# Performance work log

Measured on AMD Instinct MI355X. Metric: run time of the kernel, lower is better.

Reference implementation:

```python
import jax, jax.numpy as jnp
import numpy as np

K = 7
G = 16
PAD = K // 2
EPS = 1e-5


def setup_inputs() -> dict:
    key = jax.random.key(0)
    ks = jax.random.split(key, 8)
    C = 256
    Cr = C // 4  # ratio=4 bottleneck
    inputs = jax.random.normal(ks[0], (4, C, 56, 56), dtype=jnp.float32)
    W1 = jax.random.normal(ks[1], (Cr, C), dtype=jnp.float32) * 0.05
    b1 = jax.random.normal(ks[2], (Cr,), dtype=jnp.float32) * 0.05
    gamma = jax.random.normal(ks[3], (Cr,), dtype=jnp.float32) * 0.1 + 1.0
    beta = jax.random.normal(ks[4], (Cr,), dtype=jnp.float32) * 0.1
    mean = jax.random.normal(ks[5], (Cr,), dtype=jnp.float32) * 0.1
    var = jax.random.uniform(ks[6], (Cr,), dtype=jnp.float32) * 0.5 + 0.5
    W2 = jax.random.normal(ks[7], (G * K * K, Cr), dtype=jnp.float32) * 0.05
    b2 = jnp.zeros((G * K * K,), dtype=jnp.float32)
    return {"inputs": inputs, "W1": W1, "b1": b1, "gamma": gamma,
            "beta": beta, "mean": mean, "var": var, "W2": W2, "b2": b2}


def reference(inputs, W1, b1, gamma, beta, mean, var, W2, b2):
    B, C, H, W = inputs.shape
    Cg = C // G
    # kernel-generation branch: 1x1 conv -> BN (eval stats) -> relu -> 1x1 conv
    t = jnp.einsum('bchw,oc->bohw', inputs, W1) + b1[None, :, None, None]
    scale = gamma / jnp.sqrt(var + EPS)
    t = t * scale[None, :, None, None] + (beta - mean * scale)[None, :, None, None]
    t = jax.nn.relu(t)
    w = jnp.einsum('bchw,oc->bohw', t, W2) + b2[None, :, None, None]
    w = w.reshape(B, G, K * K, H, W)  # per-pixel kernel
    # involution: accumulate shifted slices instead of materializing unfold
    xp = jnp.pad(inputs, ((0, 0), (0, 0), (PAD, PAD), (PAD, PAD)))
    xg = xp.reshape(B, G, Cg, H + 2 * PAD, W + 2 * PAD)
    out = jnp.zeros((B, G, Cg, H, W), dtype=inputs.dtype)
    k = 0
    for i in range(K):
        for j in range(K):
            out = out + xg[:, :, :, i:i + H, j:j + W] * w[:, :, k][:, :, None, :, :]
            k += 1
    return out.reshape(B, C, H, W)
```

## Files before the change

kernel.cpp:

```cpp
#include <hip/hip_runtime.h>

#define HW    3136
#define HDIM  56
#define CIN   256
#define CR    64
#define NG    16
#define KK    49
#define BEPS  1e-5f
#define RB    2
#define NBAND 28
#define WSTR  116
#define XROWS 8
#define XSTR  68
#define XTOT  (XROWS * 8 * XSTR)

typedef __attribute__((ext_vector_type(8))) short short8;
typedef __attribute__((ext_vector_type(4))) float f32x4;

__device__ __forceinline__ unsigned short f2bf(float f) {
    union { float f; unsigned u; } v; v.f = f;
    unsigned r = (v.u + 0x7FFFu + ((v.u >> 16) & 1u)) >> 16;
    return (unsigned short)r;
}

__global__ __launch_bounds__(256) void k0_prep(
    const float* __restrict__ W1, const float* __restrict__ b1,
    const float* __restrict__ gamma, const float* __restrict__ beta,
    const float* __restrict__ mean, const float* __restrict__ var,
    const float* __restrict__ W2,
    unsigned short* __restrict__ W1b, unsigned short* __restrict__ W2bT,
    float* __restrict__ b1f)
{
    int idx = blockIdx.x * 256 + threadIdx.x;
    if (idx < CR * CIN) {
        int o = idx >> 8;
        float s = gamma[o] * rsqrtf(var[o] + BEPS);
        W1b[idx] = f2bf(W1[idx] * s);
    } else if (idx < CR * CIN + NG * 64 * 64) {
        int j = idx - CR * CIN;
        int c = j & 63, tap = (j >> 6) & 63, g = j >> 12;
        float v = (tap < KK) ? W2[(g * KK + tap) * CR + c] : 0.f;
        W2bT[j] = f2bf(v);
    } else if (idx < CR * CIN + NG * 64 * 64 + CR) {
        int o = idx - CR * CIN - NG * 64 * 64;
        float s = gamma[o] * rsqrtf(var[o] + BEPS);
        b1f[o] = b1[o] * s + beta[o] - mean[o] * s;
    }
}

__global__ __launch_bounds__(256) void k1_gemm(
    const float* __restrict__ x, const unsigned short* __restrict__ W1b,
    const float* __restrict__ b1f, unsigned short* __restrict__ t_bf)
{
    const int tid = threadIdx.x;
    const int b = blockIdx.y;
    const int lane = tid & 63, l15 = lane & 15, q = lane >> 4;
    const int wid = tid >> 6;
    const int pxb = blockIdx.x * 64 + wid * 16;

    const float* xp = x + (size_t)b * CIN * HW + pxb + l15;

    f32x4 acc[4];
#pragma unroll
    for (int nt = 0; nt < 4; nt++) acc[nt] = (f32x4){0.f, 0.f, 0.f, 0.f};

#pragma unroll 2
    for (int kc = 0; kc < 8; kc++) {
        short8 af;
#pragma unroll
        for (int j = 0; j < 8; j++) {
            float xv = xp[(size_t)(kc * 32 + q * 8 + j) * HW];
            af[j] = (short)f2bf(xv);
        }
#pragma unroll
        for (int nt = 0; nt < 4; nt++) {
            short8 bf = *(const short8*)&W1b[(size_t)(16 * nt + l15) * CIN + kc * 32 + q * 8];
            acc[nt] = __builtin_amdgcn_mfma_f32_16x16x32_bf16(af, bf, acc[nt], 0, 0, 0);
        }
    }
#pragma unroll
    for (int nt = 0; nt < 4; nt++) {
        float bias = b1f[16 * nt + l15];
#pragma unroll
        for (int r = 0; r < 4; r++) {
            int px = pxb + 4 * q + r;
            float v = fmaxf(acc[nt][r] + bias, 0.f);
            t_bf[((size_t)b * HW + px) * CR + 16 * nt + l15] = f2bf(v);
        }
    }
}

__global__ __launch_bounds__(256, 4) void k2_fused(
    const float* __restrict__ x, const unsigned short* __restrict__ t_bf,
    const unsigned short* __restrict__ W2bT, const float* __restrict__ b2,
    float* __restrict__ out)
{
    __shared__ float w_lds[KK * WSTR];
    __shared__ float x_lds[XTOT];

    const int tid = threadIdx.x;
    const int band = blockIdx.x, g = blockIdx.y;
    const int b = blockIdx.z >> 1, half = blockIdx.z & 1;
    const int h0 = band * RB;
    const int lane = tid & 63, l15 = lane & 15, q = lane >> 4;
    const int wid = tid >> 6;

#pragma unroll
    for (int it = 0; it < 17; it++) {
        int i = it * 256 + tid;
        int col = i % XSTR; int t2 = i / XSTR; int cg = t2 & 7; int rowx = t2 >> 3;
        int hy = h0 - 3 + rowx, xc = col - 4;
        float v = 0.f;
        if (hy >= 0 && hy < HDIM && xc >= 0 && xc < HDIM)
            v = x[((size_t)b * CIN + g * 16 + half * 8 + cg) * HW + hy * HDIM + xc];
        x_lds[i] = v;
    }

    {
        short8 bfr[4][2];
#pragma unroll
        for (int nt = 0; nt < 4; nt++)
#pragma unroll
            for (int ks = 0; ks < 2; ks++)
                bfr[nt][ks] = *(const short8*)&W2bT[((size_t)g * 64 + 16 * nt + l15) * 64 + ks * 32 + q * 8];
        float b2v[4];
#pragma unroll
        for (int nt = 0; nt < 4; nt++) {
            int tap = 16 * nt + l15;
            b2v[nt] = (tap < KK) ? b2[g * KK + tap] : 0.f;
        }
#pragma unroll
        for (int it = 0; it < 2; it++) {
            int mt = wid + it * 4;
            if (mt < 7) {
                const unsigned short* tp = &t_bf[((size_t)b * HW + h0 * HDIM + mt * 16 + l15) * CR];
                short8 a0 = *(const short8*)&tp[q * 8];
                short8 a1 = *(const short8*)&tp[32 + q * 8];
#pragma unroll
                for (int nt = 0; nt < 4; nt++) {
                    f32x4 acc = (f32x4){0.f, 0.f, 0.f, 0.f};
                    acc = __builtin_amdgcn_mfma_f32_16x16x32_bf16(a0, bfr[nt][0], acc, 0, 0, 0);
                    acc = __builtin_amdgcn_mfma_f32_16x16x32_bf16(a1, bfr[nt][1], acc, 0, 0, 0);
                    int tap = 16 * nt + l15;
                    if (tap < KK) {
                        *(float4*)&w_lds[tap * WSTR + mt * 16 + 4 * q] =
                            make_float4(acc[0] + b2v[nt], acc[1] + b2v[nt],
                                        acc[2] + b2v[nt], acc[3] + b2v[nt]);
                    }
                }
            }
        }
    }
    __syncthreads();

    if (tid < 224) {
        const int quad = tid >> 4;
        const int rem  = tid & 15;
        const int row  = rem >> 3;
        const int cg   = rem & 7;
        const int colb = quad * 4, h = h0 + row;

        float acc[4] = {0.f, 0.f, 0.f, 0.f};

#pragma unroll
        for (int di = 0; di < 7; di++) {
            float wv[7][4];
#pragma unroll
            for (int dj = 0; dj < 7; dj++) {
                float4 wq = *(const float4*)&w_lds[(di * 7 + dj) * WSTR + row * HDIM + colb];
                wv[dj][0] = wq.x; wv[dj][1] = wq.y; wv[dj][2] = wq.z; wv[dj][3] = wq.w;
            }
            const float* xr = &x_lds[((row + di) * 8 + cg) * XSTR + colb];
            float4 A  = *(const float4*)&xr[0];
            float4 Bv = *(const float4*)&xr[4];
            float4 Cv = *(const float4*)&xr[8];
            float win[12] = {A.x, A.y, A.z, A.w, Bv.x, Bv.y, Bv.z, Bv.w,
                             Cv.x, Cv.y, Cv.z, Cv.w};
#pragma unroll
            for (int dj = 0; dj < 7; dj++)
#pragma unroll
                for (int kk = 0; kk < 4; kk++)
                    acc[kk] += win[kk + dj + 1] * wv[dj][kk];
        }
        float* op = &out[((size_t)b * CIN + g * 16 + half * 8 + cg) * HW + h * HDIM + colb];
        *(float4*)op = make_float4(acc[0], acc[1], acc[2], acc[3]);
    }
}

extern "C" void kernel_launch(void* const* d_in, const int* in_sizes, int n_in,
                              void* d_out, int out_size, void* d_ws, size_t ws_size,
                              hipStream_t stream) {
    const float* x     = (const float*)d_in[0];
    const float* W1    = (const float*)d_in[1];
    const float* b1    = (const float*)d_in[2];
    const float* gamma = (const float*)d_in[3];
    const float* beta  = (const float*)d_in[4];
    const float* mean  = (const float*)d_in[5];
    const float* var   = (const float*)d_in[6];
    const float* W2    = (const float*)d_in[7];
    const float* b2    = (const float*)d_in[8];
    float* out = (float*)d_out;

    unsigned short* t_bf = (unsigned short*)d_ws;
    unsigned short* W1b  = t_bf + (size_t)4 * HW * CR;
    unsigned short* W2bT = W1b + CR * CIN;
    float* b1f           = (float*)(W2bT + NG * 64 * 64);

    int n_k0 = CR * CIN + NG * 64 * 64 + CR;
    k0_prep<<<(n_k0 + 255) / 256, 256, 0, stream>>>(
        W1, b1, gamma, beta, mean, var, W2, W1b, W2bT, b1f);

    dim3 g1(HW / 64, 4);
    k1_gemm<<<g1, 256, 0, stream>>>(x, W1b, b1f, t_bf);

    dim3 g2(NBAND, NG, 8);
    k2_fused<<<g2, 256, 0, stream>>>(x, t_bf, W2bT, b2, out);
}
```

Baseline: 132.1 us.

## Split-K the first GEMM and retile involution by column halves over all group channels

The first 1x1 conv kernel now uses 128-thread blocks of 16 pixels and splits the 256-channel reduction across two waves, combining the partial sums through LDS. This gives more blocks and more loads in flight. The fused involution kernel now tiles each band by column halves and covers all 16 channels of a group, so each generated per-pixel kernel is computed once per group instead of once per channel half. This removes duplicated weight-generation MFMA work and shrinks LDS so occupancy can rise. The cost is a block-level sync and reduction in k1, and some clamped or wasted MFMA lanes plus halo overhead in k2.

```diff
diff --git a/kernel.cpp b/kernel.cpp
--- a/kernel.cpp
+++ b/kernel.cpp
@@ -7,12 +7,15 @@
 #define NG    16
 #define KK    49
 #define BEPS  1e-5f
-#define RB    2
-#define NBAND 28
-#define WSTR  116
-#define XROWS 8
-#define XSTR  68
-#define XTOT  (XROWS * 8 * XSTR)
+
+#define RB     2
+#define NBAND  28
+#define CHALF  28
+#define WSTR   60
+#define XR     8
+#define XC     36
+#define XCG    16
+#define XTOT   (XR * XCG * XC)
 
 typedef __attribute__((ext_vector_type(8))) short short8;
 typedef __attribute__((ext_vector_type(4))) float f32x4;
@@ -48,15 +51,18 @@
     }
 }
 
-__global__ __launch_bounds__(256) void k1_gemm(
+__global__ __launch_bounds__(128) void k1_gemm(
     const float* __restrict__ x, const unsigned short* __restrict__ W1b,
     const float* __restrict__ b1f, unsigned short* __restrict__ t_bf)
 {
+    __shared__ float red[64 * 17];
+
     const int tid = threadIdx.x;
     const int b = blockIdx.y;
     const int lane = tid & 63, l15 = lane & 15, q = lane >> 4;
     const int wid = tid >> 6;
-    const int pxb = blockIdx.x * 64 + wid * 16;
+    const int pxb = blockIdx.x * 16;
+    const int kb = wid * 128;
 
     const float* xp = x + (size_t)b * CIN * HW + pxb + l15;
 
@@ -64,33 +70,44 @@
 #pragma unroll
     for (int nt = 0; nt < 4; nt++) acc[nt] = (f32x4){0.f, 0.f, 0.f, 0.f};
 
-#pragma unroll 2
-    for (int kc = 0; kc < 8; kc++) {
+#pragma unroll
+    for (int kc = 0; kc < 4; kc++) {
         short8 af;
 #pragma unroll
         for (int j = 0; j < 8; j++) {
-            float xv = xp[(size_t)(kc * 32 + q * 8 + j) * HW];
+            float xv = xp[(size_t)(kb + kc * 32 + q * 8 + j) * HW];
             af[j] = (short)f2bf(xv);
         }
 #pragma unroll
         for (int nt = 0; nt < 4; nt++) {
-            short8 bf = *(const short8*)&W1b[(size_t)(16 * nt + l15) * CIN + kc * 32 + q * 8];
+            short8 bf = *(const short8*)&W1b[(size_t)(16 * nt + l15) * CIN + kb + kc * 32 + q * 8];
             acc[nt] = __builtin_amdgcn_mfma_f32_16x16x32_bf16(af, bf, acc[nt], 0, 0, 0);
         }
     }
-#pragma unroll
-    for (int nt = 0; nt < 4; nt++) {
-        float bias = b1f[16 * nt + l15];
-#pragma unroll
-        for (int r = 0; r < 4; r++) {
-            int px = pxb + 4 * q + r;
-            float v = fmaxf(acc[nt][r] + bias, 0.f);
-            t_bf[((size_t)b * HW + px) * CR + 16 * nt + l15] = f2bf(v);
-        }
-    }
-}
-
-__global__ __launch_bounds__(256, 4) void k2_fused(
+
+    if (wid == 1) {
+#pragma unroll
+        for (int nt = 0; nt < 4; nt++)
+#pragma unroll
+            for (int r = 0; r < 4; r++)
+                red[lane * 17 + nt * 4 + r] = acc[nt][r];
+    }
+    __syncthreads();
+    if (wid == 0) {
+#pragma unroll
+        for (int nt = 0; nt < 4; nt++) {
+            float bias = b1f[16 * nt + l15];
+#pragma unroll
+            for (int r = 0; r < 4; r++) {
+                int px = pxb + 4 * q + r;
+                float v = acc[nt][r] + red[lane * 17 + nt * 4 + r] + bias;
+                t_bf[((size_t)b * HW + px) * CR + 16 * nt + l15] = f2bf(fmaxf(v, 0.f));
+            }
+        }
+    }
+}
+
+__global__ __launch_bounds__(256, 5) void k2_fused(
     const float* __restrict__ x, const unsigned short* __restrict__ t_bf,
     const unsigned short* __restrict__ W2bT, const float* __restrict__ b2,
     float* __restrict__ out)
@@ -99,20 +116,20 @@
     __shared__ float x_lds[XTOT];
 
     const int tid = threadIdx.x;
-    const int band = blockIdx.x, g = blockIdx.y;
-    const int b = blockIdx.z >> 1, half = blockIdx.z & 1;
-    const int h0 = band * RB;
+    const int band = blockIdx.x >> 1, chalf = blockIdx.x & 1;
+    const int g = blockIdx.y, b = blockIdx.z;
+    const int h0 = band * RB, c0 = chalf * CHALF;
     const int lane = tid & 63, l15 = lane & 15, q = lane >> 4;
     const int wid = tid >> 6;
 
 #pragma unroll
-    for (int it = 0; it < 17; it++) {
+    for (int it = 0; it < 18; it++) {
         int i = it * 256 + tid;
-        int col = i % XSTR; int t2 = i / XSTR; int cg = t2 & 7; int rowx = t2 >> 3;
-        int hy = h0 - 3 + rowx, xc = col - 4;
+        int col = i % XC; int t2 = i / XC; int cg = t2 & 15; int rowx = t2 >> 4;
+        int hy = h0 - 3 + rowx, xc = c0 + col - 4;
         float v = 0.f;
         if (hy >= 0 && hy < HDIM && xc >= 0 && xc < HDIM)
-            v = x[((size_t)b * CIN + g * 16 + half * 8 + cg) * HW + hy * HDIM + xc];
+            v = x[((size_t)b * CIN + g * 16 + cg) * HW + hy * HDIM + xc];
         x_lds[i] = v;
     }
 
@@ -129,35 +146,33 @@
             int tap = 16 * nt + l15;
             b2v[nt] = (tap < KK) ? b2[g * KK + tap] : 0.f;
         }
-#pragma unroll
-        for (int it = 0; it < 2; it++) {
-            int mt = wid + it * 4;
-            if (mt < 7) {
-                const unsigned short* tp = &t_bf[((size_t)b * HW + h0 * HDIM + mt * 16 + l15) * CR];
-                short8 a0 = *(const short8*)&tp[q * 8];
-                short8 a1 = *(const short8*)&tp[32 + q * 8];
-#pragma unroll
-                for (int nt = 0; nt < 4; nt++) {
-                    f32x4 acc = (f32x4){0.f, 0.f, 0.f, 0.f};
-                    acc = __builtin_amdgcn_mfma_f32_16x16x32_bf16(a0, bfr[nt][0], acc, 0, 0, 0);
-                    acc = __builtin_amdgcn_mfma_f32_16x16x32_bf16(a1, bfr[nt][1], acc, 0, 0, 0);
-                    int tap = 16 * nt + l15;
-                    if (tap < KK) {
-                        *(float4*)&w_lds[tap * WSTR + mt * 16 + 4 * q] =
-                            make_float4(acc[0] + b2v[nt], acc[1] + b2v[nt],
-                                        acc[2] + b2v[nt], acc[3] + b2v[nt]);
-                    }
-                }
+        const int row = wid >> 1, seg = wid & 1;
+        int px = (h0 + row) * HDIM + c0 + seg * 16 + l15;
+        if (px > HW - 1) px = HW - 1;
+        const unsigned short* tp = &t_bf[((size_t)b * HW + px) * CR];
+        short8 a0 = *(const short8*)&tp[q * 8];
+        short8 a1 = *(const short8*)&tp[32 + q * 8];
+        const int cl = seg * 16 + 4 * q;
+#pragma unroll
+        for (int nt = 0; nt < 4; nt++) {
+            f32x4 acc = (f32x4){0.f, 0.f, 0.f, 0.f};
+            acc = __builtin_amdgcn_mfma_f32_16x16x32_bf16(a0, bfr[nt][0], acc, 0, 0, 0);
+            acc = __builtin_amdgcn_mfma_f32_16x16x32_bf16(a1, bfr[nt][1], acc, 0, 0, 0);
+            int tap = 16 * nt + l15;
+            if (tap < KK && cl < CHALF) {
+                *(float4*)&w_lds[tap * WSTR + row * CHALF + cl] =
+                    make_float4(acc[0] + b2v[nt], acc[1] + b2v[nt],
+                                acc[2] + b2v[nt], acc[3] + b2v[nt]);
             }
         }
     }
     __syncthreads();
 
     if (tid < 224) {
-        const int quad = tid >> 4;
-        const int rem  = tid & 15;
-        const int row  = rem >> 3;
-        const int cg   = rem & 7;
+        const int cg   = tid & 15;
+        const int rq   = tid >> 4;
+        const int row  = rq & 1;
+        const int quad = rq >> 1;
         const int colb = quad * 4, h = h0 + row;
 
         float acc[4] = {0.f, 0.f, 0.f, 0.f};
@@ -167,10 +182,10 @@
             float wv[7][4];
 #pragma unroll
             for (int dj = 0; dj < 7; dj++) {
-                float4 wq = *(const float4*)&w_lds[(di * 7 + dj) * WSTR + row * HDIM + colb];
+                float4 wq = *(const float4*)&w_lds[(di * 7 + dj) * WSTR + row * CHALF + colb];
                 wv[dj][0] = wq.x; wv[dj][1] = wq.y; wv[dj][2] = wq.z; wv[dj][3] = wq.w;
             }
-            const float* xr = &x_lds[((row + di) * 8 + cg) * XSTR + colb];
+            const float* xr = &x_lds[((row + di) * 16 + cg) * XC + colb];
             float4 A  = *(const float4*)&xr[0];
             float4 Bv = *(const float4*)&xr[4];
             float4 Cv = *(const float4*)&xr[8];
@@ -182,7 +197,7 @@
                 for (int kk = 0; kk < 4; kk++)
                     acc[kk] += win[kk + dj + 1] * wv[dj][kk];
         }
-        float* op = &out[((size_t)b * CIN + g * 16 + half * 8 + cg) * HW + h * HDIM + colb];
+        float* op = &out[((size_t)b * CIN + g * 16 + cg) * HW + h * HDIM + c0 + colb];
         *(float4*)op = make_float4(acc[0], acc[1], acc[2], acc[3]);
     }
 }
@@ -210,9 +225,9 @@
     k0_prep<<<(n_k0 + 255) / 256, 256, 0, stream>>>(
         W1, b1, gamma, beta, mean, var, W2, W1b, W2bT, b1f);
 
-    dim3 g1(HW / 64, 4);
-    k1_gemm<<<g1, 256, 0, stream>>>(x, W1b, b1f, t_bf);
-
-    dim3 g2(NBAND, NG, 8);
+    dim3 g1(HW / 16, 4);
+    k1_gemm<<<g1, 128, 0, stream>>>(x, W1b, b1f, t_bf);
+
+    dim3 g2(NBAND * 2, NG, 4);
     k2_fused<<<g2, 256, 0, stream>>>(x, t_bf, W2bT, b2, out);
 }
```

New measurement: 127.9 us. -3.2%, faster.

## Fuse bottleneck GEMM into involution kernel with double-buffered async x loads

Applied to the files above, without the earlier changes.

Removes the separate first 1x1-conv kernel and its t_bf round trip through global memory. Each block now covers one row and half of the columns for one batch, computes t for its 28 pixels in LDS, then loops over all 16 groups. Per group it builds the per-pixel kernel with MFMA and runs the involution, while double-buffered global_load_lds prefetches the next group's x tile. In exchange grid parallelism drops to 448 blocks, and only 112 threads do involution work, behind two barriers per group.

```diff
diff --git a/kernel.cpp b/kernel.cpp
--- a/kernel.cpp
+++ b/kernel.cpp
@@ -7,12 +7,12 @@
 #define NG    16
 #define KK    49
 #define BEPS  1e-5f
-#define RB    2
-#define NBAND 28
-#define WSTR  116
-#define XROWS 8
-#define XSTR  68
-#define XTOT  (XROWS * 8 * XSTR)
+
+#define CHALF 28
+#define XC    36
+#define XBUF  4608
+#define WSTR  36
+#define TSTR  72
 
 typedef __attribute__((ext_vector_type(8))) short short8;
 typedef __attribute__((ext_vector_type(4))) float f32x4;
@@ -21,6 +21,12 @@
     union { float f; unsigned u; } v; v.f = f;
     unsigned r = (v.u + 0x7FFFu + ((v.u >> 16) & 1u)) >> 16;
     return (unsigned short)r;
+}
+
+__device__ __forceinline__ void gload_lds16(const float* gp, float* lp) {
+    __builtin_amdgcn_global_load_lds(
+        (const __attribute__((address_space(1))) void*)gp,
+        (__attribute__((address_space(3))) void*)lp, 16, 0, 0);
 }
 
 __global__ __launch_bounds__(256) void k0_prep(
@@ -48,142 +54,151 @@
     }
 }
 
-__global__ __launch_bounds__(256) void k1_gemm(
+__global__ __launch_bounds__(256, 3) void k2_fused(
     const float* __restrict__ x, const unsigned short* __restrict__ W1b,
-    const float* __restrict__ b1f, unsigned short* __restrict__ t_bf)
+    const float* __restrict__ b1f, const unsigned short* __restrict__ W2bT,
+    const float* __restrict__ b2, float* __restrict__ out)
 {
+    __shared__ unsigned short t_lds[32 * TSTR];
+    __shared__ float w_lds[KK * WSTR];
+    __shared__ float x_lds[2 * XBUF];
+
     const int tid = threadIdx.x;
-    const int b = blockIdx.y;
     const int lane = tid & 63, l15 = lane & 15, q = lane >> 4;
     const int wid = tid >> 6;
-    const int pxb = blockIdx.x * 64 + wid * 16;
-
-    const float* xp = x + (size_t)b * CIN * HW + pxb + l15;
-
-    f32x4 acc[4];
-#pragma unroll
-    for (int nt = 0; nt < 4; nt++) acc[nt] = (f32x4){0.f, 0.f, 0.f, 0.f};
+
+    const int p   = blockIdx.x + 112 * blockIdx.y;
+    const int ord = (p & 7) * 56 + (p >> 3);
+    const int h0  = ord % 56;
+    const int cb  = ord / 56;
+    const int c0  = (cb & 1) * CHALF;
+    const int b   = cb >> 1;
+
+#pragma unroll
+    for (int k = 0; k < 9; k++)
+        *(float4*)&x_lds[(k * 256 + tid) * 4] = make_float4(0.f, 0.f, 0.f, 0.f);
+    asm volatile("s_waitcnt lgkmcnt(0)" ::: "memory");
+
+#pragma unroll
+    for (int k = 0; k < 5; k++) {
+        int i = wid + 4 * k;
+        if (i < 18) {
+            int slot = i * 64 + lane;
+            int s = slot % 9, rc = slot / 9;
+            int cg = rc & 15, rowx = rc >> 4;
+            int hy = h0 - 3 + rowx, gx = c0 + 4 * s - 4;
+            if (rowx < 7 && hy >= 0 && hy < HDIM && gx >= 0 && gx <= HDIM - 4)
+                gload_lds16(&x[((size_t)b * CIN + cg) * HW + hy * HDIM + gx],
+                            &x_lds[i * 256]);
+        }
+    }
+
+    if (wid < 2) {
+        int col = wid * 16 + l15; if (col > 27) col = 27;
+        const float* xp = x + (size_t)b * CIN * HW + h0 * HDIM + c0 + col;
+        f32x4 acc[4];
+#pragma unroll
+        for (int nt = 0; nt < 4; nt++) acc[nt] = (f32x4){0.f, 0.f, 0.f, 0.f};
+#pragma unroll
+        for (int kc = 0; kc < 8; kc++) {
+            short8 af;
+#pragma unroll
+            for (int j = 0; j < 8; j++)
+                af[j] = (short)f2bf(xp[(size_t)(kc * 32 + q * 8 + j) * HW]);
+#pragma unroll
+            for (int nt = 0; nt < 4; nt++) {
+                short8 bf = *(const short8*)&W1b[(size_t)(16 * nt + l15) * CIN + kc * 32 + q * 8];
+                acc[nt] = __builtin_amdgcn_mfma_f32_16x16x32_bf16(af, bf, acc[nt], 0, 0, 0);
+            }
+        }
+#pragma unroll
+        for (int nt = 0; nt < 4; nt++) {
+            float bias = b1f[16 * nt + l15];
+#pragma unroll
+            for (int r = 0; r < 4; r++) {
+                float v = fmaxf(acc[nt][r] + bias, 0.f);
+                t_lds[(wid * 16 + 4 * q + r) * TSTR + 16 * nt + l15] = f2bf(v);
+            }
+        }
+    }
+    __syncthreads();
 
 #pragma unroll 2
-    for (int kc = 0; kc < 8; kc++) {
-        short8 af;
-#pragma unroll
-        for (int j = 0; j < 8; j++) {
-            float xv = xp[(size_t)(kc * 32 + q * 8 + j) * HW];
-            af[j] = (short)f2bf(xv);
-        }
-#pragma unroll
-        for (int nt = 0; nt < 4; nt++) {
-            short8 bf = *(const short8*)&W1b[(size_t)(16 * nt + l15) * CIN + kc * 32 + q * 8];
-            acc[nt] = __builtin_amdgcn_mfma_f32_16x16x32_bf16(af, bf, acc[nt], 0, 0, 0);
-        }
-    }
-#pragma unroll
-    for (int nt = 0; nt < 4; nt++) {
-        float bias = b1f[16 * nt + l15];
-#pragma unroll
-        for (int r = 0; r < 4; r++) {
-            int px = pxb + 4 * q + r;
-            float v = fmaxf(acc[nt][r] + bias, 0.f);
-            t_bf[((size_t)b * HW + px) * CR + 16 * nt + l15] = f2bf(v);
-        }
-    }
-}
-
-__global__ __launch_bounds__(256, 4) void k2_fused(
-    const float* __restrict__ x, const unsigned short* __restrict__ t_bf,
-    const unsigned short* __restrict__ W2bT, const float* __restrict__ b2,
-    float* __restrict__ out)
-{
-    __shared__ float w_lds[KK * WSTR];
-    __shared__ float x_lds[XTOT];
-
-    const int tid = threadIdx.x;
-    const int band = blockIdx.x, g = blockIdx.y;
-    const int b = blockIdx.z >> 1, half = blockIdx.z & 1;
-    const int h0 = band * RB;
-    const int lane = tid & 63, l15 = lane & 15, q = lane >> 4;
-    const int wid = tid >> 6;
-
-#pragma unroll
-    for (int it = 0; it < 17; it++) {
-        int i = it * 256 + tid;
-        int col = i % XSTR; int t2 = i / XSTR; int cg = t2 & 7; int rowx = t2 >> 3;
-        int hy = h0 - 3 + rowx, xc = col - 4;
-        float v = 0.f;
-        if (hy >= 0 && hy < HDIM && xc >= 0 && xc < HDIM)
-            v = x[((size_t)b * CIN + g * 16 + half * 8 + cg) * HW + hy * HDIM + xc];
-        x_lds[i] = v;
-    }
-
-    {
-        short8 bfr[4][2];
-#pragma unroll
-        for (int nt = 0; nt < 4; nt++)
-#pragma unroll
-            for (int ks = 0; ks < 2; ks++)
-                bfr[nt][ks] = *(const short8*)&W2bT[((size_t)g * 64 + 16 * nt + l15) * 64 + ks * 32 + q * 8];
-        float b2v[4];
-#pragma unroll
-        for (int nt = 0; nt < 4; nt++) {
-            int tap = 16 * nt + l15;
-            b2v[nt] = (tap < KK) ? b2[g * KK + tap] : 0.f;
-        }
-#pragma unroll
-        for (int it = 0; it < 2; it++) {
-            int mt = wid + it * 4;
-            if (mt < 7) {
-                const unsigned short* tp = &t_bf[((size_t)b * HW + h0 * HDIM + mt * 16 + l15) * CR];
-                short8 a0 = *(const short8*)&tp[q * 8];
-                short8 a1 = *(const short8*)&tp[32 + q * 8];
-#pragma unroll
-                for (int nt = 0; nt < 4; nt++) {
-                    f32x4 acc = (f32x4){0.f, 0.f, 0.f, 0.f};
-                    acc = __builtin_amdgcn_mfma_f32_16x16x32_bf16(a0, bfr[nt][0], acc, 0, 0, 0);
-                    acc = __builtin_amdgcn_mfma_f32_16x16x32_bf16(a1, bfr[nt][1], acc, 0, 0, 0);
-                    int tap = 16 * nt + l15;
-                    if (tap < KK) {
-                        *(float4*)&w_lds[tap * WSTR + mt * 16 + 4 * q] =
-                            make_float4(acc[0] + b2v[nt], acc[1] + b2v[nt],
-                                        acc[2] + b2v[nt], acc[3] + b2v[nt]);
-                    }
+    for (int g = 0; g < NG; ++g) {
+        const int buf = (g & 1) * XBUF;
+
+        if (wid < 2) {
+            short8 bfr[4][2];
+#pragma unroll
+            for (int nt = 0; nt < 4; nt++)
+#pragma unroll
+                for (int ks = 0; ks < 2; ks++)
+                    bfr[nt][ks] = *(const short8*)&W2bT[((size_t)g * 64 + 16 * nt + l15) * 64 + ks * 32 + q * 8];
+            float b2v[4];
+#pragma unroll
+            for (int nt = 0; nt < 4; nt++) {
+                int tap = 16 * nt + l15;
+                b2v[nt] = (tap < KK) ? b2[g * KK + tap] : 0.f;
+            }
+            short8 a0 = *(const short8*)&t_lds[(wid * 16 + l15) * TSTR + q * 8];
+            short8 a1 = *(const short8*)&t_lds[(wid * 16 + l15) * TSTR + 32 + q * 8];
+            const int c4 = wid * 16 + 4 * q;
+#pragma unroll
+            for (int nt = 0; nt < 4; nt++) {
+                f32x4 acc = (f32x4){0.f, 0.f, 0.f, 0.f};
+                acc = __builtin_amdgcn_mfma_f32_16x16x32_bf16(a0, bfr[nt][0], acc, 0, 0, 0);
+                acc = __builtin_amdgcn_mfma_f32_16x16x32_bf16(a1, bfr[nt][1], acc, 0, 0, 0);
+                int tap = 16 * nt + l15;
+                if (tap < KK && c4 < CHALF)
+                    *(float4*)&w_lds[tap * WSTR + c4] =
+                        make_float4(acc[0] + b2v[nt], acc[1] + b2v[nt],
+                                    acc[2] + b2v[nt], acc[3] + b2v[nt]);
+            }
+        }
+        __syncthreads();
+
+        if (tid < 112) {
+            const int cg = tid & 15, quad = tid >> 4;
+            const int colb = quad * 4;
+            float acc[4] = {0.f, 0.f, 0.f, 0.f};
+#pragma unroll
+            for (int di = 0; di < 7; di++) {
+                float wv[7][4];
+#pragma unroll
+                for (int dj = 0; dj < 7; dj++) {
+                    float4 wq = *(const float4*)&w_lds[(di * 7 + dj) * WSTR + colb];
+                    wv[dj][0] = wq.x; wv[dj][1] = wq.y; wv[dj][2] = wq.z; wv[dj][3] = wq.w;
                 }
-            }
-        }
-    }
-    __syncthreads();
-
-    if (tid < 224) {
-        const int quad = tid >> 4;
-        const int rem  = tid & 15;
-        const int row  = rem >> 3;
-        const int cg   = rem & 7;
-        const int colb = quad * 4, h = h0 + row;
-
-        float acc[4] = {0.f, 0.f, 0.f, 0.f};
-
-#pragma unroll
-        for (int di = 0; di < 7; di++) {
-            float wv[7][4];
-#pragma unroll
-            for (int dj = 0; dj < 7; dj++) {
-                float4 wq = *(const float4*)&w_lds[(di * 7 + dj) * WSTR + row * HDIM + colb];
-                wv[dj][0] = wq.x; wv[dj][1] = wq.y; wv[dj][2] = wq.z; wv[dj][3] = wq.w;
-            }
-            const float* xr = &x_lds[((row + di) * 8 + cg) * XSTR + colb];
-            float4 A  = *(const float4*)&xr[0];
-            float4 Bv = *(const float4*)&xr[4];
-            float4 Cv = *(const float4*)&xr[8];
-            float win[12] = {A.x, A.y, A.z, A.w, Bv.x, Bv.y, Bv.z, Bv.w,
-                             Cv.x, Cv.y, Cv.z, Cv.w};
-#pragma unroll
-            for (int dj = 0; dj < 7; dj++)
-#pragma unroll
-                for (int kk = 0; kk < 4; kk++)
-                    acc[kk] += win[kk + dj + 1] * wv[dj][kk];
-        }
-        float* op = &out[((size_t)b * CIN + g * 16 + half * 8 + cg) * HW + h * HDIM + colb];
-        *(float4*)op = make_float4(acc[0], acc[1], acc[2], acc[3]);
+                const float* xr = &x_lds[buf + (di * 16 + cg) * XC + colb];
+                float4 A  = *(const float4*)&xr[0];
+                float4 Bv = *(const float4*)&xr[4];
+                float4 Cv = *(const float4*)&xr[8];
+                float win[12] = {A.x, A.y, A.z, A.w, Bv.x, Bv.y, Bv.z, Bv.w,
+                                 Cv.x, Cv.y, Cv.z, Cv.w};
+#pragma unroll
+                for (int dj = 0; dj < 7; dj++)
+#pragma unroll
+                    for (int kk = 0; kk < 4; kk++)
+                        acc[kk] += win[kk + dj + 1] * wv[dj][kk];
+            }
+            float* op = &out[((size_t)b * CIN + g * 16 + cg) * HW + h0 * HDIM + c0 + colb];
+            *(float4*)op = make_float4(acc[0], acc[1], acc[2], acc[3]);
+        } else if (wid >= 2 && g + 1 < NG) {
+            const int nbuf = ((g + 1) & 1) * XBUF;
+            const int wid2 = wid - 2;
+#pragma unroll
+            for (int k = 0; k < 9; k++) {
+                int i = wid2 + 2 * k;
+                int slot = i * 64 + lane;
+                int s = slot % 9, rc = slot / 9;
+                int cg = rc & 15, rowx = rc >> 4;
+                int hy = h0 - 3 + rowx, gx = c0 + 4 * s - 4;
+                if (rowx < 7 && hy >= 0 && hy < HDIM && gx >= 0 && gx <= HDIM - 4)
+                    gload_lds16(&x[((size_t)b * CIN + (g + 1) * 16 + cg) * HW + hy * HDIM + gx],
+                                &x_lds[nbuf + i * 256]);
+            }
+        }
+        __syncthreads();
     }
 }
 
@@ -201,8 +216,7 @@
     const float* b2    = (const float*)d_in[8];
     float* out = (float*)d_out;
 
-    unsigned short* t_bf = (unsigned short*)d_ws;
-    unsigned short* W1b  = t_bf + (size_t)4 * HW * CR;
+    unsigned short* W1b  = (unsigned short*)d_ws;
     unsigned short* W2bT = W1b + CR * CIN;
     float* b1f           = (float*)(W2bT + NG * 64 * 64);
 
@@ -210,9 +224,6 @@
     k0_prep<<<(n_k0 + 255) / 256, 256, 0, stream>>>(
         W1, b1, gamma, beta, mean, var, W2, W1b, W2bT, b1f);
 
-    dim3 g1(HW / 64, 4);
-    k1_gemm<<<g1, 256, 0, stream>>>(x, W1b, b1f, t_bf);
-
-    dim3 g2(NBAND, NG, 8);
-    k2_fused<<<g2, 256, 0, stream>>>(x, t_bf, W2bT, b2, out);
-}
+    dim3 g2(112, 4);
+    k2_fused<<<g2, 256, 0, stream>>>(x, W1b, b1f, W2bT, b2, out);
+}
```

After: 123.4 us. 6.6% less time.
